# Performance work log

Measured on AMD Instinct MI355X. Metric: run time of the kernel, lower is better.

The kernel has to match this reference:

```python
import jax, jax.numpy as jnp
import numpy as np

B, S, F, E, C = 8, 8192, 512, 128, 1000


def setup_inputs() -> dict:
    key = jax.random.key(0)
    k1, k2, k3, k4 = jax.random.split(key, 4)
    x = jax.random.normal(k1, (B, F), dtype=jnp.float32)
    support_x = jax.random.normal(k2, (B, S, F), dtype=jnp.float32)
    support_y = jax.random.uniform(k3, (B, S, C), dtype=jnp.float32)
    # xavier_uniform on (1, F, E): gain * sqrt(6/(fan_in+fan_out))
    limit = float(np.sqrt(6.0 / (F + E)))
    proj_weight = jax.random.uniform(k4, (1, F, E), dtype=jnp.float32,
                                     minval=-limit, maxval=limit)
    return {"x": x, "support_x": support_x, "support_y": support_y,
            "proj_weight": proj_weight}


def reference(x, support_x, support_y, proj_weight):
    W = proj_weight[0]  # (F, E); bmm with repeated weight == shared matmul
    xq = x @ W                               # (B, E) query embedding
    sx = jnp.einsum('bsf,fe->bse', support_x, W)  # (B, S, E)
    # euclidean kernel: scores = -||xq - sx||_2, shape (B, S)
    diff = xq[:, None, :] - sx               # (B, S, E)
    scores = -jnp.sqrt(jnp.sum(diff * diff, axis=-1))
    probs = jax.nn.softmax(scores, axis=-1)  # (B, S)
    out = jnp.einsum('bs,bsc->bc', probs, support_y)  # (B, C)
    return out
```

## Files before the change

kernel.cpp:

```cpp
#include <hip/hip_runtime.h>
#include <hip/hip_bf16.h>

#define BB 8
#define SS 8192
#define FF 512
#define EE 128
#define CC 1000

typedef __bf16 bf16x8 __attribute__((ext_vector_type(8)));
typedef float  f32x4  __attribute__((ext_vector_type(4)));

__global__ void k0_wt(const float* __restrict__ W, __bf16* __restrict__ Wt) {
    int idx = blockIdx.x * 256 + threadIdx.x;
    int e = idx & (EE - 1);
    int f = idx >> 7;
    Wt[e * FF + f] = (__bf16)W[f * EE + e];
}

__global__ __launch_bounds__(256) void k_fused(
    const float* __restrict__ x,
    const float* __restrict__ sx,
    const __bf16* __restrict__ Wt,
    const float* __restrict__ y,
    float* __restrict__ pout,
    float* __restrict__ pden)
{
    __shared__ __bf16 lA[2][4][128][8];
    __shared__ __bf16 lB[2][4][128][8];
    __shared__ float  scp[2][128];
    __shared__ float  wv[128];

    const int tid   = threadIdx.x;
    const int b     = blockIdx.x >> 6;
    const int chunk = blockIdx.x & 63;
    const int srow0 = chunk << 7;
    const float* Xb = sx + ((size_t)b * SS + srow0) * FF;
    const float* xb = x + b * FF;

    const int row  = tid >> 1;
    const int kh   = tid & 1;
    const int lane = tid & 63;
    const int w    = tid >> 6;
    const int wrow = (w >> 1) * 64;
    const int wcol = (w & 1) * 64;
    const int lg   = lane >> 4;
    const int lr   = lane & 15;

    f32x4 acc[4][4];
    #pragma unroll
    for (int m = 0; m < 4; m++)
        #pragma unroll
        for (int n = 0; n < 4; n++) { f32x4 z = {0.f, 0.f, 0.f, 0.f}; acc[m][n] = z; }

    float4 sReg[4], xReg[4];

    auto LOADT = [&](int t) {
        const float* pS = Xb + (size_t)row * FF + t * 32 + kh * 16;
        const float* pX = xb + t * 32 + kh * 16;
        #pragma unroll
        for (int i = 0; i < 4; i++) {
            sReg[i] = *(const float4*)(pS + 4 * i);
            xReg[i] = *(const float4*)(pX + 4 * i);
        }
    };
    auto WRITET = [&](int buf) {
        __bf16 d[16];
        #pragma unroll
        for (int i = 0; i < 4; i++) {
            d[4 * i + 0] = (__bf16)(xReg[i].x - sReg[i].x);
            d[4 * i + 1] = (__bf16)(xReg[i].y - sReg[i].y);
            d[4 * i + 2] = (__bf16)(xReg[i].z - sReg[i].z);
            d[4 * i + 3] = (__bf16)(xReg[i].w - sReg[i].w);
        }
        *(bf16x8*)&lA[buf][kh * 2 + 0][row][0] = *(bf16x8*)&d[0];
        *(bf16x8*)&lA[buf][kh * 2 + 1][row][0] = *(bf16x8*)&d[8];
    };
    auto STAGEB = [&](int buf, int t) {
        const __bf16* pW = Wt + (size_t)row * FF + t * 32 + kh * 16;
        bf16x8 w0 = *(const bf16x8*)(pW);
        bf16x8 w1 = *(const bf16x8*)(pW + 8);
        *(bf16x8*)&lB[buf][kh * 2 + 0][row][0] = w0;
        *(bf16x8*)&lB[buf][kh * 2 + 1][row][0] = w1;
    };

    LOADT(0);
    STAGEB(0, 0);
    WRITET(0);
    __syncthreads();

    for (int t = 0; t < 16; t++) {
        const int cur = t & 1;
        if (t < 15) {
            LOADT(t + 1);
            STAGEB(cur ^ 1, t + 1);
        }
        bf16x8 af[4], bfr[4];
        #pragma unroll
        for (int m = 0; m < 4; m++)
            af[m] = *(const bf16x8*)&lA[cur][lg][wrow + m * 16 + lr][0];
        #pragma unroll
        for (int n = 0; n < 4; n++)
            bfr[n] = *(const bf16x8*)&lB[cur][lg][wcol + n * 16 + lr][0];
        #pragma unroll
        for (int m = 0; m < 4; m++)
            #pragma unroll
            for (int n = 0; n < 4; n++)
                acc[m][n] = __builtin_amdgcn_mfma_f32_16x16x32_bf16(af[m], bfr[n], acc[m][n], 0, 0, 0);
        if (t < 15) WRITET(cur ^ 1);
        __syncthreads();
    }

    float rp[4][4];
    #pragma unroll
    for (int m = 0; m < 4; m++)
        #pragma unroll
        for (int j = 0; j < 4; j++) {
            float s = 0.f;
            #pragma unroll
            for (int n = 0; n < 4; n++) { float v = acc[m][n][j]; s += v * v; }
            rp[m][j] = s;
        }
    #pragma unroll
    for (int mask = 1; mask < 16; mask <<= 1)
        #pragma unroll
        for (int m = 0; m < 4; m++)
            #pragma unroll
            for (int j = 0; j < 4; j++)
                rp[m][j] += __shfl_xor(rp[m][j], mask);

    if (lr == 0) {
        #pragma unroll
        for (int m = 0; m < 4; m++)
            #pragma unroll
            for (int j = 0; j < 4; j++)
                scp[w & 1][wrow + m * 16 + lg * 4 + j] = rp[m][j];
    }
    __syncthreads();
    if (tid < 128)
        wv[tid] = expf(-sqrtf(scp[0][tid] + scp[1][tid]));
    __syncthreads();

    if (w == 0) {
        float d = wv[lane] + wv[lane + 64];
        #pragma unroll
        for (int mask = 1; mask < 64; mask <<= 1)
            d += __shfl_xor(d, mask);
        if (lane == 0) pden[b * 64 + chunk] = d;
    }

    if (tid < 250) {
        float a0 = 0.f, a1 = 0.f, a2 = 0.f, a3 = 0.f;
        const float* base = y + ((size_t)b * SS + srow0) * CC + tid * 4;
        #pragma unroll 4
        for (int r = 0; r < 128; r++) {
            float4 v = *(const float4*)(base + (size_t)r * CC);
            float wgt = wv[r];
            a0 += wgt * v.x; a1 += wgt * v.y; a2 += wgt * v.z; a3 += wgt * v.w;
        }
        float4 res = {a0, a1, a2, a3};
        *(float4*)(pout + ((size_t)(b * 64 + chunk)) * CC + tid * 4) = res;
    }
}

__global__ void k4_final(const float* __restrict__ pout, const float* __restrict__ pden,
                         float* __restrict__ out) {
    int idx = blockIdx.x * 256 + threadIdx.x;
    if (idx >= BB * CC) return;
    int b = idx / CC, c = idx % CC;
    float den = 0.f;
    #pragma unroll 8
    for (int k = 0; k < 64; k++) den += pden[b * 64 + k];
    float num = 0.f;
    #pragma unroll 8
    for (int k = 0; k < 64; k++) num += pout[((size_t)(b * 64 + k)) * CC + c];
    out[idx] = num / den;
}

extern "C" void kernel_launch(void* const* d_in, const int* in_sizes, int n_in,
                              void* d_out, int out_size, void* d_ws, size_t ws_size,
                              hipStream_t stream) {
    const float* x  = (const float*)d_in[0];
    const float* sx = (const float*)d_in[1];
    const float* sy = (const float*)d_in[2];
    const float* W  = (const float*)d_in[3];

    char* ws = (char*)d_ws;
    __bf16* Wt   = (__bf16*)(ws);
    float*  pout = (float*)(ws + 131072);
    float*  pden = (float*)(ws + 131072 + 2048000);

    k0_wt<<<256, 256, 0, stream>>>(W, Wt);
    k_fused<<<512, 256, 0, stream>>>(x, sx, Wt, sy, pout, pden);
    k4_final<<<32, 256, 0, stream>>>(pout, pden, (float*)d_out);
}
```

Measured before the change: 89.17 us.

## Deepen support_x prefetch to two tiles and prefetch support_y rows early

The GEMM main loop now keeps two alternating register sets for support_x so global loads are issued two k-tiles ahead, and the W tile is held in registers and written to LDS together with the difference tile. The loop is fully unrolled. The first 8 support_y rows are loaded before the score reduction, and the weighted-sum loop prefetches the next 8 rows while accumulating. The goal is to hide global memory latency in a bandwidth-bound kernel, at the cost of many more live registers, which may lower occupancy or cause spills.

```diff
diff --git a/kernel.cpp b/kernel.cpp
--- a/kernel.cpp
+++ b/kernel.cpp
@@ -52,62 +52,102 @@
         #pragma unroll
         for (int n = 0; n < 4; n++) { f32x4 z = {0.f, 0.f, 0.f, 0.f}; acc[m][n] = z; }
 
-    float4 sReg[4], xReg[4];
-
-    auto LOADT = [&](int t) {
-        const float* pS = Xb + (size_t)row * FF + t * 32 + kh * 16;
-        const float* pX = xb + t * 32 + kh * 16;
+    float4 sA[4], sB[4];
+    float4 xReg[4];
+    bf16x8 bReg0, bReg1;
+
+    auto LOADS_A = [&](int t) {
+        const float* p = Xb + (size_t)row * FF + t * 32 + kh * 16;
+        #pragma unroll
+        for (int i = 0; i < 4; i++) sA[i] = *(const float4*)(p + 4 * i);
+    };
+    auto LOADS_B = [&](int t) {
+        const float* p = Xb + (size_t)row * FF + t * 32 + kh * 16;
+        #pragma unroll
+        for (int i = 0; i < 4; i++) sB[i] = *(const float4*)(p + 4 * i);
+    };
+    auto LOADX = [&](int t) {
+        const float* p = xb + t * 32 + kh * 16;
+        #pragma unroll
+        for (int i = 0; i < 4; i++) xReg[i] = *(const float4*)(p + 4 * i);
+    };
+    auto LOADB = [&](int t) {
+        const __bf16* pW = Wt + (size_t)row * FF + t * 32 + kh * 16;
+        bReg0 = *(const bf16x8*)(pW);
+        bReg1 = *(const bf16x8*)(pW + 8);
+    };
+    auto WRITE_FROM_A = [&](int buf) {
+        __bf16 d[16];
         #pragma unroll
         for (int i = 0; i < 4; i++) {
-            sReg[i] = *(const float4*)(pS + 4 * i);
-            xReg[i] = *(const float4*)(pX + 4 * i);
-        }
-    };
-    auto WRITET = [&](int buf) {
+            d[4*i+0] = (__bf16)(xReg[i].x - sA[i].x);
+            d[4*i+1] = (__bf16)(xReg[i].y - sA[i].y);
+            d[4*i+2] = (__bf16)(xReg[i].z - sA[i].z);
+            d[4*i+3] = (__bf16)(xReg[i].w - sA[i].w);
+        }
+        *(bf16x8*)&lA[buf][kh*2+0][row][0] = *(bf16x8*)&d[0];
+        *(bf16x8*)&lA[buf][kh*2+1][row][0] = *(bf16x8*)&d[8];
+        *(bf16x8*)&lB[buf][kh*2+0][row][0] = bReg0;
+        *(bf16x8*)&lB[buf][kh*2+1][row][0] = bReg1;
+    };
+    auto WRITE_FROM_B = [&](int buf) {
         __bf16 d[16];
         #pragma unroll
         for (int i = 0; i < 4; i++) {
-            d[4 * i + 0] = (__bf16)(xReg[i].x - sReg[i].x);
-            d[4 * i + 1] = (__bf16)(xReg[i].y - sReg[i].y);
-            d[4 * i + 2] = (__bf16)(xReg[i].z - sReg[i].z);
-            d[4 * i + 3] = (__bf16)(xReg[i].w - sReg[i].w);
-        }
-        *(bf16x8*)&lA[buf][kh * 2 + 0][row][0] = *(bf16x8*)&d[0];
-        *(bf16x8*)&lA[buf][kh * 2 + 1][row][0] = *(bf16x8*)&d[8];
-    };
-    auto STAGEB = [&](int buf, int t) {
-        const __bf16* pW = Wt + (size_t)row * FF + t * 32 + kh * 16;
-        bf16x8 w0 = *(const bf16x8*)(pW);
-        bf16x8 w1 = *(const bf16x8*)(pW + 8);
-        *(bf16x8*)&lB[buf][kh * 2 + 0][row][0] = w0;
-        *(bf16x8*)&lB[buf][kh * 2 + 1][row][0] = w1;
-    };
-
-    LOADT(0);
-    STAGEB(0, 0);
-    WRITET(0);
+            d[4*i+0] = (__bf16)(xReg[i].x - sB[i].x);
+            d[4*i+1] = (__bf16)(xReg[i].y - sB[i].y);
+            d[4*i+2] = (__bf16)(xReg[i].z - sB[i].z);
+            d[4*i+3] = (__bf16)(xReg[i].w - sB[i].w);
+        }
+        *(bf16x8*)&lA[buf][kh*2+0][row][0] = *(bf16x8*)&d[0];
+        *(bf16x8*)&lA[buf][kh*2+1][row][0] = *(bf16x8*)&d[8];
+        *(bf16x8*)&lB[buf][kh*2+0][row][0] = bReg0;
+        *(bf16x8*)&lB[buf][kh*2+1][row][0] = bReg1;
+    };
+    auto MFMA_STEP = [&](int buf) {
+        bf16x8 af[4], bfr[4];
+        #pragma unroll
+        for (int m = 0; m < 4; m++)
+            af[m] = *(const bf16x8*)&lA[buf][lg][wrow + m * 16 + lr][0];
+        #pragma unroll
+        for (int n = 0; n < 4; n++)
+            bfr[n] = *(const bf16x8*)&lB[buf][lg][wcol + n * 16 + lr][0];
+        #pragma unroll
+        for (int m = 0; m < 4; m++)
+            #pragma unroll
+            for (int n = 0; n < 4; n++)
+                acc[m][n] = __builtin_amdgcn_mfma_f32_16x16x32_bf16(af[m], bfr[n], acc[m][n], 0, 0, 0);
+    };
+
+    LOADS_A(0);
+    LOADS_B(1);
+    LOADX(0);
+    LOADB(0);
+    WRITE_FROM_A(0);
     __syncthreads();
 
+    #pragma unroll
     for (int t = 0; t < 16; t++) {
         const int cur = t & 1;
-        if (t < 15) {
-            LOADT(t + 1);
-            STAGEB(cur ^ 1, t + 1);
-        }
-        bf16x8 af[4], bfr[4];
-        #pragma unroll
-        for (int m = 0; m < 4; m++)
-            af[m] = *(const bf16x8*)&lA[cur][lg][wrow + m * 16 + lr][0];
-        #pragma unroll
-        for (int n = 0; n < 4; n++)
-            bfr[n] = *(const bf16x8*)&lB[cur][lg][wcol + n * 16 + lr][0];
-        #pragma unroll
-        for (int m = 0; m < 4; m++)
-            #pragma unroll
-            for (int n = 0; n < 4; n++)
-                acc[m][n] = __builtin_amdgcn_mfma_f32_16x16x32_bf16(af[m], bfr[n], acc[m][n], 0, 0, 0);
-        if (t < 15) WRITET(cur ^ 1);
+        if (t + 2 < 16) {
+            if ((t & 1) == 0) LOADS_A(t + 2);
+            else              LOADS_B(t + 2);
+        }
+        if (t + 1 < 16) { LOADX(t + 1); LOADB(t + 1); }
+        MFMA_STEP(cur);
+        if (t + 1 < 16) {
+            if ((t & 1) == 0) WRITE_FROM_B(cur ^ 1);
+            else              WRITE_FROM_A(cur ^ 1);
+        }
         __syncthreads();
+    }
+
+    const float* ybase = y + ((size_t)b * SS + srow0) * CC + tid * 4;
+    float4 yReg[8];
+    if (tid < 250) {
+        #pragma unroll
+        for (int i = 0; i < 8; i++)
+            yReg[i] = *(const float4*)(ybase + (size_t)i * CC);
     }
 
     float rp[4][4];
@@ -150,12 +190,15 @@
 
     if (tid < 250) {
         float a0 = 0.f, a1 = 0.f, a2 = 0.f, a3 = 0.f;
-        const float* base = y + ((size_t)b * SS + srow0) * CC + tid * 4;
-        #pragma unroll 4
-        for (int r = 0; r < 128; r++) {
-            float4 v = *(const float4*)(base + (size_t)r * CC);
-            float wgt = wv[r];
-            a0 += wgt * v.x; a1 += wgt * v.y; a2 += wgt * v.z; a3 += wgt * v.w;
+        for (int r0 = 0; r0 < 128; r0 += 8) {
+            #pragma unroll
+            for (int i = 0; i < 8; i++) {
+                float4 v = yReg[i];
+                float wgt = wv[r0 + i];
+                a0 += wgt * v.x; a1 += wgt * v.y; a2 += wgt * v.z; a3 += wgt * v.w;
+                if (r0 + 8 + i < 128)
+                    yReg[i] = *(const float4*)(ybase + (size_t)(r0 + 8 + i) * CC);
+            }
         }
         float4 res = {a0, a1, a2, a3};
         *(float4*)(pout + ((size_t)(b * 64 + chunk)) * CC + tid * 4) = res;
```

After: 91.82 us. 1.03x slower.

## Load MFMA operands directly from global into registers, dropping LDS staging

Applied to the files above, without the earlier changes.

The GEMM main loop no longer stages the difference tile and weights through shared memory. Each lane now loads its MFMA fragment rows of support_x, x and Wt straight from global memory into double-buffered registers, and the kernel requests two blocks per CU through launch bounds. This removes the LDS writes and reads and the per-iteration barriers. In exchange, the global loads are less coalesced: each lane reads 32-byte pieces from strided rows, and each wave redundantly loads Wt and the x values. Register pressure also goes up, which may cause spills under the 2-block occupancy target.

```diff
diff --git a/kernel.cpp b/kernel.cpp
--- a/kernel.cpp
+++ b/kernel.cpp
@@ -17,7 +17,7 @@
     Wt[e * FF + f] = (__bf16)W[f * EE + e];
 }
 
-__global__ __launch_bounds__(256) void k_fused(
+__global__ __launch_bounds__(256, 2) void k_fused(
     const float* __restrict__ x,
     const float* __restrict__ sx,
     const __bf16* __restrict__ Wt,
@@ -25,20 +25,14 @@
     float* __restrict__ pout,
     float* __restrict__ pden)
 {
-    __shared__ __bf16 lA[2][4][128][8];
-    __shared__ __bf16 lB[2][4][128][8];
-    __shared__ float  scp[2][128];
-    __shared__ float  wv[128];
+    __shared__ float scp[2][128];
+    __shared__ float wv[128];
 
     const int tid   = threadIdx.x;
     const int b     = blockIdx.x >> 6;
     const int chunk = blockIdx.x & 63;
     const int srow0 = chunk << 7;
-    const float* Xb = sx + ((size_t)b * SS + srow0) * FF;
-    const float* xb = x + b * FF;
 
-    const int row  = tid >> 1;
-    const int kh   = tid & 1;
     const int lane = tid & 63;
     const int w    = tid >> 6;
     const int wrow = (w >> 1) * 64;
@@ -46,68 +40,68 @@
     const int lg   = lane >> 4;
     const int lr   = lane & 15;
 
+    const float* Arow[4];
+    #pragma unroll
+    for (int m = 0; m < 4; m++)
+        Arow[m] = sx + ((size_t)b * SS + srow0 + wrow + m * 16 + lr) * FF + lg * 8;
+    const __bf16* Bcol[4];
+    #pragma unroll
+    for (int n = 0; n < 4; n++)
+        Bcol[n] = Wt + (size_t)(wcol + n * 16 + lr) * FF + lg * 8;
+    const float* xp = x + b * FF + lg * 8;
+
     f32x4 acc[4][4];
     #pragma unroll
     for (int m = 0; m < 4; m++)
         #pragma unroll
         for (int n = 0; n < 4; n++) { f32x4 z = {0.f, 0.f, 0.f, 0.f}; acc[m][n] = z; }
 
-    float4 sReg[4], xReg[4];
+    float4 sE[4][2], sO[4][2], xE[2], xO[2];
+    bf16x8 bE[4], bO[4];
 
-    auto LOADT = [&](int t) {
-        const float* pS = Xb + (size_t)row * FF + t * 32 + kh * 16;
-        const float* pX = xb + t * 32 + kh * 16;
-        #pragma unroll
-        for (int i = 0; i < 4; i++) {
-            sReg[i] = *(const float4*)(pS + 4 * i);
-            xReg[i] = *(const float4*)(pX + 4 * i);
-        }
-    };
-    auto WRITET = [&](int buf) {
-        __bf16 d[16];
-        #pragma unroll
-        for (int i = 0; i < 4; i++) {
-            d[4 * i + 0] = (__bf16)(xReg[i].x - sReg[i].x);
-            d[4 * i + 1] = (__bf16)(xReg[i].y - sReg[i].y);
-            d[4 * i + 2] = (__bf16)(xReg[i].z - sReg[i].z);
-            d[4 * i + 3] = (__bf16)(xReg[i].w - sReg[i].w);
-        }
-        *(bf16x8*)&lA[buf][kh * 2 + 0][row][0] = *(bf16x8*)&d[0];
-        *(bf16x8*)&lA[buf][kh * 2 + 1][row][0] = *(bf16x8*)&d[8];
-    };
-    auto STAGEB = [&](int buf, int t) {
-        const __bf16* pW = Wt + (size_t)row * FF + t * 32 + kh * 16;
-        bf16x8 w0 = *(const bf16x8*)(pW);
-        bf16x8 w1 = *(const bf16x8*)(pW + 8);
-        *(bf16x8*)&lB[buf][kh * 2 + 0][row][0] = w0;
-        *(bf16x8*)&lB[buf][kh * 2 + 1][row][0] = w1;
-    };
-
-    LOADT(0);
-    STAGEB(0, 0);
-    WRITET(0);
-    __syncthreads();
-
-    for (int t = 0; t < 16; t++) {
-        const int cur = t & 1;
-        if (t < 15) {
-            LOADT(t + 1);
-            STAGEB(cur ^ 1, t + 1);
-        }
-        bf16x8 af[4], bfr[4];
+    auto LOADSET = [&](int t, float4 (&sS)[4][2], float4 (&xS)[2], bf16x8 (&bS)[4]) {
         #pragma unroll
         for (int m = 0; m < 4; m++)
-            af[m] = *(const bf16x8*)&lA[cur][lg][wrow + m * 16 + lr][0];
+            #pragma unroll
+            for (int h = 0; h < 2; h++)
+                sS[m][h] = *(const float4*)(Arow[m] + t * 32 + h * 4);
+        #pragma unroll
+        for (int h = 0; h < 2; h++)
+            xS[h] = *(const float4*)(xp + t * 32 + h * 4);
         #pragma unroll
         for (int n = 0; n < 4; n++)
-            bfr[n] = *(const bf16x8*)&lB[cur][lg][wcol + n * 16 + lr][0];
+            bS[n] = *(const bf16x8*)(Bcol[n] + t * 32);
+    };
+    auto COMPUTE = [&](float4 (&sS)[4][2], float4 (&xS)[2], bf16x8 (&bS)[4]) {
+        bf16x8 af[4];
+        #pragma unroll
+        for (int m = 0; m < 4; m++) {
+            __bf16 d[8];
+            #pragma unroll
+            for (int h = 0; h < 2; h++) {
+                d[4*h+0] = (__bf16)(xS[h].x - sS[m][h].x);
+                d[4*h+1] = (__bf16)(xS[h].y - sS[m][h].y);
+                d[4*h+2] = (__bf16)(xS[h].z - sS[m][h].z);
+                d[4*h+3] = (__bf16)(xS[h].w - sS[m][h].w);
+            }
+            af[m] = *(bf16x8*)d;
+        }
         #pragma unroll
         for (int m = 0; m < 4; m++)
             #pragma unroll
             for (int n = 0; n < 4; n++)
-                acc[m][n] = __builtin_amdgcn_mfma_f32_16x16x32_bf16(af[m], bfr[n], acc[m][n], 0, 0, 0);
-        if (t < 15) WRITET(cur ^ 1);
-        __syncthreads();
+                acc[m][n] = __builtin_amdgcn_mfma_f32_16x16x32_bf16(af[m], bS[n], acc[m][n], 0, 0, 0);
+    };
+
+    LOADSET(0, sE, xE, bE);
+    #pragma unroll
+    for (int t = 0; t < 16; t++) {
+        if (t + 1 < 16) {
+            if (t & 1) LOADSET(t + 1, sE, xE, bE);
+            else       LOADSET(t + 1, sO, xO, bO);
+        }
+        if (t & 1) COMPUTE(sO, xO, bO);
+        else       COMPUTE(sE, xE, bE);
     }
 
     float rp[4][4];
```

Result: slower. 120.4 us (+35.0%).

## Process two chunks per block, overlapping chunk0 y-reduction with chunk1 GEMM

Applied to the files above, without the earlier changes.

Each block now handles two 128-row chunks of the support set. The y-weighted accumulation for the first chunk is interleaved with the MFMA loop of the second chunk, using double-buffered y register loads, and a relaxed barrier that only waits on LDS counters. The aim is to hide the y streaming latency behind matrix work. The cost is half as many blocks, which lowers occupancy, plus higher register pressure, and the second chunk's y pass still runs serially.

```diff
diff --git a/kernel.cpp b/kernel.cpp
--- a/kernel.cpp
+++ b/kernel.cpp
@@ -9,6 +9,11 @@
 
 typedef __bf16 bf16x8 __attribute__((ext_vector_type(8)));
 typedef float  f32x4  __attribute__((ext_vector_type(4)));
+
+#define BAR_RELAXED() do { \
+    asm volatile("s_waitcnt lgkmcnt(0)" ::: "memory"); \
+    __builtin_amdgcn_s_barrier(); \
+} while (0)
 
 __global__ void k0_wt(const float* __restrict__ W, __bf16* __restrict__ Wt) {
     int idx = blockIdx.x * 256 + threadIdx.x;
@@ -28,14 +33,17 @@
     __shared__ __bf16 lA[2][4][128][8];
     __shared__ __bf16 lB[2][4][128][8];
     __shared__ float  scp[2][128];
-    __shared__ float  wv[128];
-
-    const int tid   = threadIdx.x;
-    const int b     = blockIdx.x >> 6;
-    const int chunk = blockIdx.x & 63;
-    const int srow0 = chunk << 7;
-    const float* Xb = sx + ((size_t)b * SS + srow0) * FF;
-    const float* xb = x + b * FF;
+    __shared__ float  wv[2][128];
+
+    const int tid  = threadIdx.x;
+    const int bid  = blockIdx.x;
+    const int b    = bid >> 5;
+    const int pair = bid & 31;
+    const int c0   = pair * 2;
+    const int c1   = pair * 2 + 1;
+    const float* Xb0 = sx + ((size_t)b * SS + (c0 << 7)) * FF;
+    const float* Xb1 = sx + ((size_t)b * SS + (c1 << 7)) * FF;
+    const float* xb  = x + b * FF;
 
     const int row  = tid >> 1;
     const int kh   = tid & 1;
@@ -47,14 +55,15 @@
     const int lr   = lane & 15;
 
     f32x4 acc[4][4];
-    #pragma unroll
-    for (int m = 0; m < 4; m++)
-        #pragma unroll
-        for (int n = 0; n < 4; n++) { f32x4 z = {0.f, 0.f, 0.f, 0.f}; acc[m][n] = z; }
-
     float4 sReg[4], xReg[4];
 
-    auto LOADT = [&](int t) {
+    auto ZEROACC = [&]() {
+        #pragma unroll
+        for (int m = 0; m < 4; m++)
+            #pragma unroll
+            for (int n = 0; n < 4; n++) { f32x4 z = {0.f, 0.f, 0.f, 0.f}; acc[m][n] = z; }
+    };
+    auto LOADT = [&](const float* Xb, int t) {
         const float* pS = Xb + (size_t)row * FF + t * 32 + kh * 16;
         const float* pX = xb + t * 32 + kh * 16;
         #pragma unroll
@@ -67,98 +76,152 @@
         __bf16 d[16];
         #pragma unroll
         for (int i = 0; i < 4; i++) {
-            d[4 * i + 0] = (__bf16)(xReg[i].x - sReg[i].x);
-            d[4 * i + 1] = (__bf16)(xReg[i].y - sReg[i].y);
-            d[4 * i + 2] = (__bf16)(xReg[i].z - sReg[i].z);
-            d[4 * i + 3] = (__bf16)(xReg[i].w - sReg[i].w);
-        }
-        *(bf16x8*)&lA[buf][kh * 2 + 0][row][0] = *(bf16x8*)&d[0];
-        *(bf16x8*)&lA[buf][kh * 2 + 1][row][0] = *(bf16x8*)&d[8];
+            d[4*i+0] = (__bf16)(xReg[i].x - sReg[i].x);
+            d[4*i+1] = (__bf16)(xReg[i].y - sReg[i].y);
+            d[4*i+2] = (__bf16)(xReg[i].z - sReg[i].z);
+            d[4*i+3] = (__bf16)(xReg[i].w - sReg[i].w);
+        }
+        *(bf16x8*)&lA[buf][kh*2+0][row][0] = *(bf16x8*)&d[0];
+        *(bf16x8*)&lA[buf][kh*2+1][row][0] = *(bf16x8*)&d[8];
     };
     auto STAGEB = [&](int buf, int t) {
         const __bf16* pW = Wt + (size_t)row * FF + t * 32 + kh * 16;
         bf16x8 w0 = *(const bf16x8*)(pW);
         bf16x8 w1 = *(const bf16x8*)(pW + 8);
-        *(bf16x8*)&lB[buf][kh * 2 + 0][row][0] = w0;
-        *(bf16x8*)&lB[buf][kh * 2 + 1][row][0] = w1;
-    };
-
-    LOADT(0);
-    STAGEB(0, 0);
-    WRITET(0);
+        *(bf16x8*)&lB[buf][kh*2+0][row][0] = w0;
+        *(bf16x8*)&lB[buf][kh*2+1][row][0] = w1;
+    };
+    auto MFMA_STEP = [&](int buf) {
+        bf16x8 af[4], bfr[4];
+        #pragma unroll
+        for (int m = 0; m < 4; m++)
+            af[m] = *(const bf16x8*)&lA[buf][lg][wrow + m * 16 + lr][0];
+        #pragma unroll
+        for (int n = 0; n < 4; n++)
+            bfr[n] = *(const bf16x8*)&lB[buf][lg][wcol + n * 16 + lr][0];
+        #pragma unroll
+        for (int m = 0; m < 4; m++)
+            #pragma unroll
+            for (int n = 0; n < 4; n++)
+                acc[m][n] = __builtin_amdgcn_mfma_f32_16x16x32_bf16(af[m], bfr[n], acc[m][n], 0, 0, 0);
+    };
+    auto EPILOGUE = [&](int which, int chunk) {
+        float rp[4][4];
+        #pragma unroll
+        for (int m = 0; m < 4; m++)
+            #pragma unroll
+            for (int j = 0; j < 4; j++) {
+                float s = 0.f;
+                #pragma unroll
+                for (int n = 0; n < 4; n++) { float v = acc[m][n][j]; s += v * v; }
+                rp[m][j] = s;
+            }
+        #pragma unroll
+        for (int mask = 1; mask < 16; mask <<= 1)
+            #pragma unroll
+            for (int m = 0; m < 4; m++)
+                #pragma unroll
+                for (int j = 0; j < 4; j++)
+                    rp[m][j] += __shfl_xor(rp[m][j], mask);
+        if (lr == 0) {
+            #pragma unroll
+            for (int m = 0; m < 4; m++)
+                #pragma unroll
+                for (int j = 0; j < 4; j++)
+                    scp[w & 1][wrow + m * 16 + lg * 4 + j] = rp[m][j];
+        }
+        __syncthreads();
+        if (tid < 128)
+            wv[which][tid] = expf(-sqrtf(scp[0][tid] + scp[1][tid]));
+        __syncthreads();
+        if (w == 0) {
+            float d = wv[which][lane] + wv[which][lane + 64];
+            #pragma unroll
+            for (int mask = 1; mask < 64; mask <<= 1)
+                d += __shfl_xor(d, mask);
+            if (lane == 0) pden[b * 64 + chunk] = d;
+        }
+    };
+
+    ZEROACC();
+    LOADT(Xb0, 0); STAGEB(0, 0); WRITET(0);
     __syncthreads();
-
     for (int t = 0; t < 16; t++) {
         const int cur = t & 1;
-        if (t < 15) {
-            LOADT(t + 1);
-            STAGEB(cur ^ 1, t + 1);
-        }
-        bf16x8 af[4], bfr[4];
-        #pragma unroll
-        for (int m = 0; m < 4; m++)
-            af[m] = *(const bf16x8*)&lA[cur][lg][wrow + m * 16 + lr][0];
-        #pragma unroll
-        for (int n = 0; n < 4; n++)
-            bfr[n] = *(const bf16x8*)&lB[cur][lg][wcol + n * 16 + lr][0];
-        #pragma unroll
-        for (int m = 0; m < 4; m++)
-            #pragma unroll
-            for (int n = 0; n < 4; n++)
-                acc[m][n] = __builtin_amdgcn_mfma_f32_16x16x32_bf16(af[m], bfr[n], acc[m][n], 0, 0, 0);
+        if (t < 15) { LOADT(Xb0, t + 1); STAGEB(cur ^ 1, t + 1); }
+        MFMA_STEP(cur);
         if (t < 15) WRITET(cur ^ 1);
         __syncthreads();
     }
-
-    float rp[4][4];
+    EPILOGUE(0, c0);
+
+    ZEROACC();
+    const bool act = (tid < 250);
+    const float* yb0 = y + ((size_t)b * SS + (c0 << 7)) * CC + tid * 4;
+    const float* yb1 = y + ((size_t)b * SS + (c1 << 7)) * CC + tid * 4;
+    float4 yA[8], yB[8];
+    float a0 = 0.f, a1 = 0.f, a2 = 0.f, a3 = 0.f;
+
+    LOADT(Xb1, 0); STAGEB(0, 0); WRITET(0);
+    if (act) {
+        #pragma unroll
+        for (int i = 0; i < 8; i++) yA[i] = *(const float4*)(yb0 + (size_t)i * CC);
+    }
+    __syncthreads();
+
     #pragma unroll
-    for (int m = 0; m < 4; m++)
-        #pragma unroll
-        for (int j = 0; j < 4; j++) {
-            float s = 0.f;
-            #pragma unroll
-            for (int n = 0; n < 4; n++) { float v = acc[m][n][j]; s += v * v; }
-            rp[m][j] = s;
-        }
-    #pragma unroll
-    for (int mask = 1; mask < 16; mask <<= 1)
-        #pragma unroll
-        for (int m = 0; m < 4; m++)
-            #pragma unroll
-            for (int j = 0; j < 4; j++)
-                rp[m][j] += __shfl_xor(rp[m][j], mask);
-
-    if (lr == 0) {
-        #pragma unroll
-        for (int m = 0; m < 4; m++)
-            #pragma unroll
-            for (int j = 0; j < 4; j++)
-                scp[w & 1][wrow + m * 16 + lg * 4 + j] = rp[m][j];
-    }
-    __syncthreads();
-    if (tid < 128)
-        wv[tid] = expf(-sqrtf(scp[0][tid] + scp[1][tid]));
-    __syncthreads();
-
-    if (w == 0) {
-        float d = wv[lane] + wv[lane + 64];
-        #pragma unroll
-        for (int mask = 1; mask < 64; mask <<= 1)
-            d += __shfl_xor(d, mask);
-        if (lane == 0) pden[b * 64 + chunk] = d;
-    }
-
-    if (tid < 250) {
-        float a0 = 0.f, a1 = 0.f, a2 = 0.f, a3 = 0.f;
-        const float* base = y + ((size_t)b * SS + srow0) * CC + tid * 4;
-        #pragma unroll 4
+    for (int t = 0; t < 16; t++) {
+        const int cur = t & 1;
+        if (t < 15) { LOADT(Xb1, t + 1); STAGEB(cur ^ 1, t + 1); }
+        if (t + 1 < 16 && act) {
+            if ((t + 1) & 1) {
+                #pragma unroll
+                for (int i = 0; i < 8; i++)
+                    yB[i] = *(const float4*)(yb0 + (size_t)(8 * (t + 1) + i) * CC);
+            } else {
+                #pragma unroll
+                for (int i = 0; i < 8; i++)
+                    yA[i] = *(const float4*)(yb0 + (size_t)(8 * (t + 1) + i) * CC);
+            }
+        }
+        MFMA_STEP(cur);
+        if (act) {
+            if (t & 1) {
+                #pragma unroll
+                for (int i = 0; i < 8; i++) {
+                    float wgt = wv[0][8 * t + i];
+                    a0 += wgt * yB[i].x; a1 += wgt * yB[i].y;
+                    a2 += wgt * yB[i].z; a3 += wgt * yB[i].w;
+                }
+            } else {
+                #pragma unroll
+                for (int i = 0; i < 8; i++) {
+                    float wgt = wv[0][8 * t + i];
+                    a0 += wgt * yA[i].x; a1 += wgt * yA[i].y;
+                    a2 += wgt * yA[i].z; a3 += wgt * yA[i].w;
+                }
+            }
+        }
+        if (t < 15) WRITET(cur ^ 1);
+        BAR_RELAXED();
+    }
+    if (act) {
+        float4 res = {a0, a1, a2, a3};
+        *(float4*)(pout + ((size_t)(b * 64 + c0)) * CC + tid * 4) = res;
+    }
+
+    EPILOGUE(1, c1);
+
+    if (act) {
+        float e0 = 0.f, e1 = 0.f, e2 = 0.f, e3 = 0.f;
+        #pragma unroll 8
         for (int r = 0; r < 128; r++) {
-            float4 v = *(const float4*)(base + (size_t)r * CC);
-            float wgt = wv[r];
-            a0 += wgt * v.x; a1 += wgt * v.y; a2 += wgt * v.z; a3 += wgt * v.w;
-        }
-        float4 res = {a0, a1, a2, a3};
-        *(float4*)(pout + ((size_t)(b * 64 + chunk)) * CC + tid * 4) = res;
+            float4 v = *(const float4*)(yb1 + (size_t)r * CC);
+            float wgt = wv[1][r];
+            e0 += wgt * v.x; e1 += wgt * v.y; e2 += wgt * v.z; e3 += wgt * v.w;
+        }
+        float4 res = {e0, e1, e2, e3};
+        *(float4*)(pout + ((size_t)(b * 64 + c1)) * CC + tid * 4) = res;
     }
 }
 
@@ -190,6 +253,6 @@
     float*  pden = (float*)(ws + 131072 + 2048000);
 
     k0_wt<<<256, 256, 0, stream>>>(W, Wt);
-    k_fused<<<512, 256, 0, stream>>>(x, sx, Wt, sy, pout, pden);
+    k_fused<<<256, 256, 0, stream>>>(x, sx, Wt, sy, pout, pden);
     k4_final<<<32, 256, 0, stream>>>(pout, pden, (float*)d_out);
 }
```

Result: slower. 97.19 us (+9.0%).
